# Kernel tuning notes

Hardware: AMD Instinct MI355X
Metric: run time of the kernel (lower is better)

Reference implementation:

```python
import jax, jax.numpy as jnp
from jax import lax
import numpy as np

N = 1024
REG_FG_THRESH = 0.55   # UNLABELED_REG_FG_THRESH
CLS_FG_THRESH = 0.75
CLS_BG_THRESH = 0.25
NMS_THRESH = 0.1
EPS = 1e-8


def _cross2(a, b):
    return a[..., 0] * b[..., 1] - a[..., 1] * b[..., 0]


def _box_corners(box):  # box [7] -> BEV corners [4,2]
    c = box[0:2]
    dx, dy, r = box[3], box[4], box[6]
    tmpl = jnp.array([[0.5, 0.5], [0.5, -0.5], [-0.5, -0.5], [-0.5, 0.5]], dtype=box.dtype)
    local = tmpl * jnp.stack([dx, dy])
    cs, sn = jnp.cos(r), jnp.sin(r)
    rot = jnp.stack([local[:, 0] * cs - local[:, 1] * sn,
                     local[:, 0] * sn + local[:, 1] * cs], axis=1)
    return rot + c


def _pts_in_box(pts, box):  # pts [K,2] -> bool [K]
    d = pts - box[0:2]
    cs, sn = jnp.cos(-box[6]), jnp.sin(-box[6])
    lx = d[:, 0] * cs - d[:, 1] * sn
    ly = d[:, 0] * sn + d[:, 1] * cs
    return (jnp.abs(lx) <= box[3] * 0.5 + 1e-5) & (jnp.abs(ly) <= box[4] * 0.5 + 1e-5)


def _rect_inter_area(ba, bb):
    # intersection area of two rotated BEV rectangles (convex polygon clip)
    ca = _box_corners(ba); cb = _box_corners(bb)
    in_b = _pts_in_box(ca, bb); in_a = _pts_in_box(cb, ba)
    a0, a1 = ca, jnp.roll(ca, -1, 0)
    b0, b1 = cb, jnp.roll(cb, -1, 0)
    d1 = (a1 - a0)[:, None, :]; d2 = (b1 - b0)[None, :, :]
    r0 = b0[None, :, :] - a0[:, None, :]
    den = _cross2(d1, d2)
    sden = jnp.where(jnp.abs(den) < EPS, 1.0, den)
    t = _cross2(r0, d2) / sden
    u = _cross2(r0, d1) / sden
    ok = (jnp.abs(den) > EPS) & (t >= 0) & (t <= 1) & (u >= 0) & (u <= 1)
    ipts = a0[:, None, :] + t[..., None] * d1          # [4,4,2]
    pts = jnp.concatenate([ca, cb, ipts.reshape(16, 2)], 0)   # [24,2]
    valid = jnp.concatenate([in_b, in_a, ok.reshape(16)], 0)
    k = valid.sum()
    ctr = (pts * valid[:, None]).sum(0) / jnp.maximum(k, 1)
    cen = jnp.where(valid[:, None], pts - ctr, 0.0)
    ang = jnp.where(valid, jnp.arctan2(cen[:, 1], cen[:, 0]), 1e9)
    p = cen[jnp.argsort(ang)]                          # valid verts first, CCW order
    idx = jnp.arange(24)
    nxt = jnp.where(idx + 1 < k, idx + 1, 0)
    cr = p[idx, 0] * p[nxt, 1] - p[idx, 1] * p[nxt, 0]
    area = 0.5 * jnp.abs(jnp.sum(jnp.where(idx < k, cr, 0.0)))
    return jnp.where(k >= 3, area, 0.0)


_pairwise_inter = jax.vmap(jax.vmap(_rect_inter_area, (None, 0)), (0, None))  # [N,M]


def boxes_iou_bev(a, b):
    inter = _pairwise_inter(a, b)
    sa = (a[:, 3] * a[:, 4])[:, None]
    sb = (b[:, 3] * b[:, 4])[None, :]
    return inter / jnp.clip(sa + sb - inter, EPS, None)


def boxes_iou3d(a, b):
    inter_bev = _pairwise_inter(a, b)
    amax = (a[:, 2] + a[:, 5] * 0.5)[:, None]; amin = (a[:, 2] - a[:, 5] * 0.5)[:, None]
    bmax = (b[:, 2] + b[:, 5] * 0.5)[None, :]; bmin = (b[:, 2] - b[:, 5] * 0.5)[None, :]
    oh = jnp.clip(jnp.minimum(amax, bmax) - jnp.maximum(amin, bmin), 0.0, None)
    inter3d = inter_bev * oh
    va = (a[:, 3] * a[:, 4] * a[:, 5])[:, None]
    vb = (b[:, 3] * b[:, 4] * b[:, 5])[None, :]
    return inter3d / jnp.clip(va + vb - inter3d, EPS, None)


def nms_bev(boxes, scores, thresh):
    # greedy rotated-BEV NMS (OpenPCDet nms_gpu semantics), returns keep mask [N]
    n = boxes.shape[0]
    order = jnp.argsort(-scores)
    iou_o = boxes_iou_bev(boxes, boxes)[order][:, order]
    ar = jnp.arange(n)
    def body(i, keep):
        sup = (iou_o[i] > thresh) & (ar > i) & keep[i]
        return keep & ~sup
    keep = lax.fori_loop(0, n, body, jnp.ones((n,), bool))
    return jnp.zeros((n,), bool).at[order].set(keep)


def _make_boxes(k, n):
    ka, kb, kc, kd = jax.random.split(k, 4)
    xy = jax.random.uniform(ka, (n, 2), minval=-40.0, maxval=40.0)
    z = jax.random.uniform(kb, (n, 1), minval=-2.0, maxval=0.0)
    dims = jax.random.uniform(kc, (n, 3), minval=1.0, maxval=5.0)
    ry = jax.random.uniform(kd, (n, 1), minval=-np.pi, maxval=np.pi)
    return jnp.concatenate([xy, z, dims, ry], axis=1)


def setup_inputs() -> dict:
    key = jax.random.key(0)
    k1, k2, k3, k4, k5, k6, k7 = jax.random.split(key, 7)
    pred_boxes = _make_boxes(k1, N)
    gt7 = _make_boxes(k2, N)
    # place gt boxes near predictions so IoUs are non-trivial
    gt7 = gt7.at[:, :3].set(pred_boxes[:, :3] + jax.random.normal(k3, (N, 3)) * 0.5)
    gt_labels = jax.random.randint(k4, (N, 1), 1, 4).astype(jnp.float32)
    gt_boxes = jnp.concatenate([gt7, gt_labels], axis=1)  # [N,8]
    return {
        'rcnn_cls_labels': jax.random.uniform(k5, (N,), dtype=jnp.float32),
        'pred_boxes': pred_boxes,
        'gt_boxes': gt_boxes,
        'rcnn_cls': jax.random.normal(k6, (N,), dtype=jnp.float32),
        'reg_valid_mask': jax.random.randint(k7, (N,), 0, 2).astype(jnp.int64),
    }


def reference(rcnn_cls_labels, pred_boxes, gt_boxes, rcnn_cls, reg_valid_mask):
    # --- filtering mask -> reg_valid_mask (shape [1,N] via unsqueeze(0), as in torch) ---
    cls_preds = jax.nn.sigmoid(rcnn_cls)[None]                       # [1,N]
    filtering = (cls_preds > REG_FG_THRESH) & (rcnn_cls_labels[None] > REG_FG_THRESH)
    reg_valid = filtering.astype(jnp.int32)
    # --- NMS on gt (pseudo) boxes scored by rcnn_cls_labels ---
    sampled = nms_bev(gt_boxes[:, 0:7], rcnn_cls_labels, NMS_THRESH)  # [N] bool
    gt_m = jnp.where(sampled[:, None], gt_boxes, 0.0)
    # --- IoU3D overlap + threshold-based fg/bg relabeling ---
    iou3d = boxes_iou3d(pred_boxes[:, 0:7], gt_m[:, 0:7])             # [N,N]
    max_overlaps = iou3d.max(axis=1)
    gt_assignment = jnp.argmax(iou3d, axis=1)
    max_overlaps = jnp.where(max_overlaps > CLS_FG_THRESH, 1.0,
                             jnp.where(max_overlaps < CLS_BG_THRESH, 0.0, max_overlaps))
    return reg_valid, rcnn_cls_labels, max_overlaps, gt_assignment
```

## Files before the change

kernel.cpp:

```cpp
#include <hip/hip_runtime.h>
#include <math.h>


#define NB 1024

typedef unsigned long long u64;

__device__ __forceinline__ bool pt_in_box(float px, float py,
        float bx, float by, float bdx, float bdy, float cs, float sn) {
    float dx = px - bx, dy = py - by;
    float lx = dx * cs + dy * sn;
    float ly = dy * cs - dx * sn;
    return (fabsf(lx) <= bdx * 0.5f + 1e-5f) && (fabsf(ly) <= bdy * 0.5f + 1e-5f);
}

__device__ __forceinline__ unsigned sortbits(float f) {
    unsigned u = __float_as_uint(f + 0.0f);
    return (u & 0x80000000u) ? ~u : (u | 0x80000000u);
}

__device__ float rect_inter_area(
        float ax, float ay, float adx, float ady, float ar,
        float bx, float by, float bdx, float bdy, float br) {
    float dcx = ax - bx, dcy = ay - by;
    float ra = 0.5f * sqrtf(adx * adx + ady * ady);
    float rb = 0.5f * sqrtf(bdx * bdx + bdy * bdy);
    float lim = ra + rb + 1e-3f;
    if (dcx * dcx + dcy * dcy > lim * lim) return 0.0f;

    float csa = cosf(ar), sna = sinf(ar);
    float csb = cosf(br), snb = sinf(br);
    float cax[4], cay[4], cbx[4], cby[4];
    const float SX[4] = {0.5f, 0.5f, -0.5f, -0.5f};
    const float SY[4] = {0.5f, -0.5f, -0.5f, 0.5f};
#pragma unroll
    for (int i = 0; i < 4; ++i) {
        float lx = SX[i] * adx, ly = SY[i] * ady;
        cax[i] = lx * csa - ly * sna + ax;
        cay[i] = lx * sna + ly * csa + ay;
        float mx = SX[i] * bdx, my = SY[i] * bdy;
        cbx[i] = mx * csb - my * snb + bx;
        cby[i] = mx * snb + my * csb + by;
    }

    unsigned vmask = 0u;
    float sx = 0.0f, sy = 0.0f;
#pragma unroll
    for (int i = 0; i < 4; ++i) {
        bool v = pt_in_box(cax[i], cay[i], bx, by, bdx, bdy, csb, snb);
        vmask |= v ? (1u << i) : 0u;
        sx += v ? cax[i] : 0.0f;
        sy += v ? cay[i] : 0.0f;
    }
#pragma unroll
    for (int i = 0; i < 4; ++i) {
        bool v = pt_in_box(cbx[i], cby[i], ax, ay, adx, ady, csa, sna);
        vmask |= v ? (1u << (4 + i)) : 0u;
        sx += v ? cbx[i] : 0.0f;
        sy += v ? cby[i] : 0.0f;
    }
#pragma unroll
    for (int i = 0; i < 4; ++i) {
        float a0x = cax[i], a0y = cay[i];
        float d1x = cax[(i + 1) & 3] - a0x, d1y = cay[(i + 1) & 3] - a0y;
#pragma unroll
        for (int j = 0; j < 4; ++j) {
            int s = 8 + i * 4 + j;
            float b0x = cbx[j], b0y = cby[j];
            float d2x = cbx[(j + 1) & 3] - b0x, d2y = cby[(j + 1) & 3] - b0y;
            float r0x = b0x - a0x, r0y = b0y - a0y;
            float den = d1x * d2y - d1y * d2x;
            bool nz = fabsf(den) > 1e-8f;
            float sden = nz ? den : 1.0f;
            float t = (r0x * d2y - r0y * d2x) / sden;
            float u = (r0x * d1y - r0y * d1x) / sden;
            bool ok = nz && t >= 0.0f && t <= 1.0f && u >= 0.0f && u <= 1.0f;
            float ipx = a0x + t * d1x;
            float ipy = a0y + t * d1y;
            vmask |= ok ? (1u << s) : 0u;
            sx += ok ? ipx : 0.0f;
            sy += ok ? ipy : 0.0f;
        }
    }
    int kc = __popc(vmask);
    if (kc < 3) return 0.0f;
    float ctrx = sx / (float)kc, ctry = sy / (float)kc;

    float cx24[24], cy24[24];
    unsigned h[24];
#pragma unroll
    for (int i = 0; i < 4; ++i) {
        {
            bool v = (vmask >> i) & 1u;
            float cx = v ? cax[i] - ctrx : 0.0f;
            float cy = v ? cay[i] - ctry : 0.0f;
            cx24[i] = cx; cy24[i] = cy;
            h[i] = sortbits(v ? atan2f(cy, cx) : 1e9f);
        }
        {
            bool v = (vmask >> (4 + i)) & 1u;
            float cx = v ? cbx[i] - ctrx : 0.0f;
            float cy = v ? cby[i] - ctry : 0.0f;
            cx24[4 + i] = cx; cy24[4 + i] = cy;
            h[4 + i] = sortbits(v ? atan2f(cy, cx) : 1e9f);
        }
    }
#pragma unroll
    for (int i = 0; i < 4; ++i) {
        float a0x = cax[i], a0y = cay[i];
        float d1x = cax[(i + 1) & 3] - a0x, d1y = cay[(i + 1) & 3] - a0y;
#pragma unroll
        for (int j = 0; j < 4; ++j) {
            int s = 8 + i * 4 + j;
            float b0x = cbx[j], b0y = cby[j];
            float d2x = cbx[(j + 1) & 3] - b0x, d2y = cby[(j + 1) & 3] - b0y;
            float r0x = b0x - a0x, r0y = b0y - a0y;
            float den = d1x * d2y - d1y * d2x;
            bool nz = fabsf(den) > 1e-8f;
            float sden = nz ? den : 1.0f;
            float t = (r0x * d2y - r0y * d2x) / sden;
            bool v = (vmask >> s) & 1u;
            float ipx = a0x + t * d1x;
            float ipy = a0y + t * d1y;
            float cx = v ? ipx - ctrx : 0.0f;
            float cy = v ? ipy - ctry : 0.0f;
            cx24[s] = cx; cy24[s] = cy;
            h[s] = sortbits(v ? atan2f(cy, cx) : 1e9f);
        }
    }

    int rk[24];
#pragma unroll
    for (int s = 0; s < 24; ++s) rk[s] = 0;
#pragma unroll
    for (int s = 0; s < 24; ++s) {
#pragma unroll
        for (int t = s + 1; t < 24; ++t) {
            bool a = h[s] <= h[t];
            rk[t] += a ? 1 : 0;
            rk[s] += a ? 0 : 1;
        }
    }

    float acc = 0.0f;
    float fx = 0.0f, fy = 0.0f, lx2 = 0.0f, ly2 = 0.0f;
    float pxp = 0.0f, pyp = 0.0f;
#pragma unroll
    for (int p = 0; p < 24; ++p) {
        float X = 0.0f, Y = 0.0f;
#pragma unroll
        for (int s = 0; s < 24; ++s) {
            bool m = (rk[s] == p);
            X = m ? cx24[s] : X;
            Y = m ? cy24[s] : Y;
        }
        if (p == 0) {
            fx = X; fy = Y;
        } else {
            float cr = pxp * Y - pyp * X;
            acc += (p < kc) ? cr : 0.0f;
        }
        bool e = (p == kc - 1);
        lx2 = e ? X : lx2;
        ly2 = e ? Y : ly2;
        pxp = X; pyp = Y;
    }
    acc += lx2 * fy - ly2 * fx;
    return 0.5f * fabsf(acc);
}

__global__ __launch_bounds__(256) void prep_sa_kernel(
        const float* __restrict__ labels, const float* __restrict__ pred,
        const float* __restrict__ gt, const float* __restrict__ cls,
        float* __restrict__ out, int* __restrict__ rankinv,
        float* __restrict__ sbox, float4* __restrict__ circ_s,
        float4* __restrict__ circ_g, float4* __restrict__ circ_p) {
    int tid = threadIdx.x;
    int lane = tid & 63;
    int e = ((int)blockIdx.x * 256 + tid) >> 6;
    float ke = labels[e];
    const float4* lab4 = (const float4*)labels;
    int cntr = 0;
#pragma unroll
    for (int kk = 0; kk < 4; ++kk) {
        float4 kv = lab4[lane * 4 + kk];
        int t0 = lane * 16 + kk * 4;
        cntr += ((kv.x > ke) || (kv.x == ke && (t0 + 0) < e)) ? 1 : 0;
        cntr += ((kv.y > ke) || (kv.y == ke && (t0 + 1) < e)) ? 1 : 0;
        cntr += ((kv.z > ke) || (kv.z == ke && (t0 + 2) < e)) ? 1 : 0;
        cntr += ((kv.w > ke) || (kv.w == ke && (t0 + 3) < e)) ? 1 : 0;
    }
#pragma unroll
    for (int off = 32; off > 0; off >>= 1) cntr += __shfl_xor(cntr, off, 64);
    int rank = cntr;
    if (lane < 7) sbox[rank * 8 + lane] = gt[e * 8 + lane];
    if (lane == 7) sbox[rank * 8 + 7] = 0.0f;
    if (lane == 0) {
        rankinv[e] = rank;
        float gdx = gt[e * 8 + 3], gdy = gt[e * 8 + 4];
        float4 cgc = make_float4(gt[e * 8 + 0], gt[e * 8 + 1],
                                 0.5f * sqrtf(gdx * gdx + gdy * gdy), 0.0f);
        circ_s[rank] = cgc;
        circ_g[e] = cgc;
        float pdx = pred[e * 7 + 3], pdy = pred[e * 7 + 4];
        circ_p[e] = make_float4(pred[e * 7 + 0], pred[e * 7 + 1],
                                0.5f * sqrtf(pdx * pdx + pdy * pdy), 0.0f);
        float sig = 1.0f / (1.0f + expf(-cls[e]));
        out[e] = (sig > 0.55f && ke > 0.55f) ? 1.0f : 0.0f;
        out[NB + e] = ke;
    }
}

__global__ __launch_bounds__(256) void supA_sa_kernel(
        const float* __restrict__ sbox, const float4* __restrict__ circ_s,
        u64* __restrict__ sup) {
    __shared__ unsigned ring[4096];
    __shared__ unsigned cnt_s;
    __shared__ unsigned sup32[128];
    int tid = threadIdx.x;
    int b = blockIdx.x;
    int lane = tid & 63;
    int wv = tid >> 6;
    if (tid == 0) cnt_s = 0u;
    for (int t = tid; t < 128; t += 256) sup32[t] = 0u;
    __syncthreads();
    {
        int i = b + (wv << 8);
        float4 A = circ_s[i];
        int j0 = ((i + 1) >> 6) << 6;
        for (int jb = j0; jb < 1024; jb += 64) {
            int j = jb + lane;
            bool q = j > i;
            if (q) {
                float4 B = circ_s[j];
                float dx = A.x - B.x, dy = A.y - B.y;
                float lim = A.z + B.z + 1e-3f;
                q = (dx * dx + dy * dy) <= lim * lim;
            }
            if (q) {
                unsigned pos = atomicAdd(&cnt_s, 1u);
                ring[pos] = (unsigned)((i << 10) | j);
            }
        }
    }
    __syncthreads();
    {
        unsigned n = cnt_s;
        for (unsigned t = tid; t < n; t += 256) {
            unsigned p = ring[t];
            int i = (p >> 10) & 1023, j = p & 1023;
            const float* A = &sbox[i * 8];
            const float* B = &sbox[j * 8];
            float inter = rect_inter_area(A[0], A[1], A[3], A[4], A[6],
                                          B[0], B[1], B[3], B[4], B[6]);
            float iou = inter / fmaxf(A[3] * A[4] + B[3] * B[4] - inter, 1e-8f);
            if (iou > 0.1f) {
                int r = (i - b) >> 8;
                atomicOr(&sup32[r * 32 + (j >> 5)], 1u << (j & 31));
            }
        }
    }
    __syncthreads();
    for (int t = tid; t < 64; t += 256) {
        int r = t >> 4, w = t & 15;
        int i = b + (r << 8);
        sup[i * 16 + w] = (u64)sup32[r * 32 + 2 * w] |
                          ((u64)sup32[r * 32 + 2 * w + 1] << 32);
    }
}

__global__ __launch_bounds__(256) void outB_fused_kernel(
        const float* __restrict__ pred, const float* __restrict__ gt,
        const int* __restrict__ rankinv, const float4* __restrict__ circ_p,
        const float4* __restrict__ circ_g, const u64* __restrict__ sup,
        float* __restrict__ out) {
    __shared__ unsigned ring[4096];
    __shared__ unsigned cnt_s;
    __shared__ u64 bc[64];
    __shared__ u64 ksh[16];
    __shared__ u64 rm[4];
    int tid = threadIdx.x;
    int b = blockIdx.x;
    int lane = tid & 63;
    int wv = tid >> 6;
    if (tid == 0) cnt_s = 0u;
    if (tid < 4) rm[tid] = 1023ULL;
    __syncthreads();

    if (tid < 64) {
        u64 acc[16];
        u64 row[16];
#pragma unroll
        for (int t = 0; t < 16; ++t) acc[t] = 0ULL;
#pragma unroll
        for (int t = 0; t < 16; ++t) row[t] = sup[(size_t)lane * 16 + t];
#pragma unroll
        for (int W = 0; W < 16; ++W) {
            u64 kwW;
            if (W == 0) {
                kwW = ~0ULL;
            } else {
                u64 v = acc[W];
#pragma unroll
                for (int off = 32; off > 0; off >>= 1)
                    v |= __shfl_xor(v, off, 64);
                kwW = ~v;
            }
            bc[lane] = row[W];
            u64 rowN[16];
#pragma unroll
            for (int t = 0; t < 16; ++t) rowN[t] = 0ULL;
            if (W < 15) {
#pragma unroll
                for (int t = 0; t < 16; ++t)
                    if (t >= W + 1)
                        rowN[t] = sup[(size_t)((W + 1) * 64 + lane) * 16 + t];
            }
#pragma unroll
            for (int g = 0; g < 4; ++g) {
                u64 rb[16];
#pragma unroll
                for (int t = 0; t < 16; ++t) rb[t] = bc[g * 16 + t];
#pragma unroll
                for (int t = 0; t < 16; ++t) {
                    int bb = g * 16 + t;
                    bool kb = (kwW >> bb) & 1ULL;
                    kwW &= kb ? ~rb[t] : ~0ULL;
                }
            }
            if (lane == 0) ksh[W] = kwW;
            bool me = (kwW >> lane) & 1ULL;
#pragma unroll
            for (int t = W + 1; t < 16; ++t) acc[t] |= me ? row[t] : 0ULL;
#pragma unroll
            for (int t = 0; t < 16; ++t) row[t] = rowN[t];
        }
    } else {
        for (int task = wv - 1; task < 64; task += 3) {
            int r = task >> 4;
            int jb = (task & 15) << 6;
            int i = b + (r << 8);
            float4 A = circ_p[i];
            int j = jb + lane;
            float4 B = circ_g[j];
            float dx = A.x - B.x, dy = A.y - B.y;
            float lim = A.z + B.z + 1e-3f;
            if (dx * dx + dy * dy <= lim * lim) {
                unsigned pos = atomicAdd(&cnt_s, 1u);
                if (pos < 4096u) ring[pos] = (unsigned)((i << 10) | j);
            }
        }
    }
    __syncthreads();

    {
        unsigned n = min(cnt_s, 4096u);
        for (unsigned t = tid; t < n; t += 256) {
            unsigned p = ring[t];
            int i = (p >> 10) & 1023, j = p & 1023;
            int rr = rankinv[j];
            if (!((ksh[rr >> 6] >> (rr & 63)) & 1ULL)) continue;
            float Ax = pred[i * 7 + 0], Ay = pred[i * 7 + 1], Az = pred[i * 7 + 2];
            float Adx = pred[i * 7 + 3], Ady = pred[i * 7 + 4], Adz = pred[i * 7 + 5];
            float Ar = pred[i * 7 + 6];
            float Bx = gt[j * 8 + 0], By = gt[j * 8 + 1], Bz = gt[j * 8 + 2];
            float Bdx = gt[j * 8 + 3], Bdy = gt[j * 8 + 4], Bdz = gt[j * 8 + 5];
            float Br = gt[j * 8 + 6];
            float inter = rect_inter_area(Ax, Ay, Adx, Ady, Ar,
                                          Bx, By, Bdx, Bdy, Br);
            float amax = Az + Adz * 0.5f, amin = Az - Adz * 0.5f;
            float bmax = Bz + Bdz * 0.5f, bmin = Bz - Bdz * 0.5f;
            float oh = fmaxf(fminf(amax, bmax) - fmaxf(amin, bmin), 0.0f);
            float inter3d = inter * oh;
            float va = Adx * Ady * Adz, vb = Bdx * Bdy * Bdz;
            float iou = inter3d / fmaxf(va + vb - inter3d, 1e-8f);
            u64 pk = (((u64)__float_as_uint(iou)) << 32) | (u64)(1023 - j);
            int r = (i - b) >> 8;
            atomicMax(&rm[r], pk);
        }
    }
    __syncthreads();
    if (tid < 4) {
        int i = b + (tid << 8);
        u64 v = rm[tid];
        float fv = __uint_as_float((unsigned)(v >> 32));
        int j = 1023 - (int)(v & 0xFFFFFFFFULL);
        float mo = (fv > 0.75f) ? 1.0f : ((fv < 0.25f) ? 0.0f : fv);
        out[2 * NB + i] = mo;
        out[3 * NB + i] = (float)j;
    }
}

extern "C" void kernel_launch(void* const* d_in, const int* in_sizes, int n_in,
                              void* d_out, int out_size, void* d_ws, size_t ws_size,
                              hipStream_t stream) {
    const float* labels = (const float*)d_in[0];
    const float* pred   = (const float*)d_in[1];
    const float* gt     = (const float*)d_in[2];
    const float* cls    = (const float*)d_in[3];
    float* out = (float*)d_out;

    char* ws = (char*)d_ws;
    int* rankinv   = (int*)ws;
    float* sbox    = (float*)(ws + 4096);
    u64* sup       = (u64*)(ws + 40960);
    float4* circ_s = (float4*)(ws + 172032);
    float4* circ_g = (float4*)(ws + 188416);
    float4* circ_p = (float4*)(ws + 204800);

    prep_sa_kernel<<<256, 256, 0, stream>>>(labels, pred, gt, cls, out,
                                            rankinv, sbox, circ_s, circ_g,
                                            circ_p);
    supA_sa_kernel<<<256, 256, 0, stream>>>(sbox, circ_s, sup);
    outB_fused_kernel<<<256, 256, 0, stream>>>(pred, gt, rankinv, circ_p,
                                               circ_g, sup, out);
}
```

Baseline: 137.6 us.

## Compute candidate IoUs speculatively in worker waves, overlapping the NMS wave

The three worker waves now compact candidate pairs into per-wave segments using ballot/popcount instead of a shared atomic counter. They then compute the 3D IoU for every candidate right away, in parallel with wave 0's serial NMS keep-mask resolution. The final pass only checks the keep mask and does atomicMax on the precomputed IoU. In exchange, IoU is computed for pairs whose gt box may later be suppressed, and only 3 of 4 waves do that work. The per-wave capacity (SEG=1408) changes the overflow behaviour and raises shared-memory use.

```diff
diff --git a/kernel.cpp b/kernel.cpp
--- a/kernel.cpp
+++ b/kernel.cpp
@@ -3,6 +3,7 @@
 
 
 #define NB 1024
+#define SEG 1408
 
 typedef unsigned long long u64;
 
@@ -167,6 +168,24 @@
     }
     acc += lx2 * fy - ly2 * fx;
     return 0.5f * fabsf(acc);
+}
+
+__device__ __forceinline__ float iou3d_pair(
+        const float* __restrict__ pred, const float* __restrict__ gt,
+        int i, int j) {
+    float Ax = pred[i * 7 + 0], Ay = pred[i * 7 + 1], Az = pred[i * 7 + 2];
+    float Adx = pred[i * 7 + 3], Ady = pred[i * 7 + 4], Adz = pred[i * 7 + 5];
+    float Ar = pred[i * 7 + 6];
+    float Bx = gt[j * 8 + 0], By = gt[j * 8 + 1], Bz = gt[j * 8 + 2];
+    float Bdx = gt[j * 8 + 3], Bdy = gt[j * 8 + 4], Bdz = gt[j * 8 + 5];
+    float Br = gt[j * 8 + 6];
+    float inter = rect_inter_area(Ax, Ay, Adx, Ady, Ar, Bx, By, Bdx, Bdy, Br);
+    float amax = Az + Adz * 0.5f, amin = Az - Adz * 0.5f;
+    float bmax = Bz + Bdz * 0.5f, bmin = Bz - Bdz * 0.5f;
+    float oh = fmaxf(fminf(amax, bmax) - fmaxf(amin, bmin), 0.0f);
+    float inter3d = inter * oh;
+    float va = Adx * Ady * Adz, vb = Bdx * Bdy * Bdz;
+    return inter3d / fmaxf(va + vb - inter3d, 1e-8f);
 }
 
 __global__ __launch_bounds__(256) void prep_sa_kernel(
@@ -274,8 +293,9 @@
         const int* __restrict__ rankinv, const float4* __restrict__ circ_p,
         const float4* __restrict__ circ_g, const u64* __restrict__ sup,
         float* __restrict__ out) {
-    __shared__ unsigned ring[4096];
-    __shared__ unsigned cnt_s;
+    __shared__ unsigned ring[3 * SEG];
+    __shared__ float fio[3 * SEG];
+    __shared__ unsigned scnt[3];
     __shared__ u64 bc[64];
     __shared__ u64 ksh[16];
     __shared__ u64 rm[4];
@@ -283,7 +303,6 @@
     int b = blockIdx.x;
     int lane = tid & 63;
     int wv = tid >> 6;
-    if (tid == 0) cnt_s = 0u;
     if (tid < 4) rm[tid] = 1023ULL;
     __syncthreads();
 
@@ -336,6 +355,8 @@
             for (int t = 0; t < 16; ++t) row[t] = rowN[t];
         }
     } else {
+        unsigned base = (unsigned)(wv - 1) * SEG;
+        unsigned mycnt = 0;
         for (int task = wv - 1; task < 64; task += 3) {
             int r = task >> 4;
             int jb = (task & 15) << 6;
@@ -345,38 +366,35 @@
             float4 B = circ_g[j];
             float dx = A.x - B.x, dy = A.y - B.y;
             float lim = A.z + B.z + 1e-3f;
-            if (dx * dx + dy * dy <= lim * lim) {
-                unsigned pos = atomicAdd(&cnt_s, 1u);
-                if (pos < 4096u) ring[pos] = (unsigned)((i << 10) | j);
-            }
-        }
-    }
-    __syncthreads();
-
-    {
-        unsigned n = min(cnt_s, 4096u);
+            bool q = (dx * dx + dy * dy) <= lim * lim;
+            u64 m = __ballot(q ? 1 : 0);
+            if (q) {
+                unsigned pos = mycnt +
+                    (unsigned)__popcll(m & ((1ULL << lane) - 1ULL));
+                ring[base + pos] = (unsigned)((i << 10) | j);
+            }
+            mycnt += (unsigned)__popcll(m);
+        }
+        if (lane == 0) scnt[wv - 1] = mycnt;
+        for (unsigned t = lane; t < mycnt; t += 64) {
+            unsigned p = ring[base + t];
+            int i = (p >> 10) & 1023, j = p & 1023;
+            fio[base + t] = iou3d_pair(pred, gt, i, j);
+        }
+    }
+    __syncthreads();
+
+#pragma unroll 1
+    for (int s = 0; s < 3; ++s) {
+        unsigned n = min(scnt[s], (unsigned)SEG);
         for (unsigned t = tid; t < n; t += 256) {
-            unsigned p = ring[t];
+            unsigned p = ring[s * SEG + t];
             int i = (p >> 10) & 1023, j = p & 1023;
             int rr = rankinv[j];
             if (!((ksh[rr >> 6] >> (rr & 63)) & 1ULL)) continue;
-            float Ax = pred[i * 7 + 0], Ay = pred[i * 7 + 1], Az = pred[i * 7 + 2];
-            float Adx = pred[i * 7 + 3], Ady = pred[i * 7 + 4], Adz = pred[i * 7 + 5];
-            float Ar = pred[i * 7 + 6];
-            float Bx = gt[j * 8 + 0], By = gt[j * 8 + 1], Bz = gt[j * 8 + 2];
-            float Bdx = gt[j * 8 + 3], Bdy = gt[j * 8 + 4], Bdz = gt[j * 8 + 5];
-            float Br = gt[j * 8 + 6];
-            float inter = rect_inter_area(Ax, Ay, Adx, Ady, Ar,
-                                          Bx, By, Bdx, Bdy, Br);
-            float amax = Az + Adz * 0.5f, amin = Az - Adz * 0.5f;
-            float bmax = Bz + Bdz * 0.5f, bmin = Bz - Bdz * 0.5f;
-            float oh = fmaxf(fminf(amax, bmax) - fmaxf(amin, bmin), 0.0f);
-            float inter3d = inter * oh;
-            float va = Adx * Ady * Adz, vb = Bdx * Bdy * Bdz;
-            float iou = inter3d / fmaxf(va + vb - inter3d, 1e-8f);
+            float iou = fio[s * SEG + t];
             u64 pk = (((u64)__float_as_uint(iou)) << 32) | (u64)(1023 - j);
-            int r = (i - b) >> 8;
-            atomicMax(&rm[r], pk);
+            atomicMax(&rm[(i - b) >> 8], pk);
         }
     }
     __syncthreads();
```

Result: faster. 115.8 us (-15.9%).
